# Performance work log

Measured on AMD Instinct MI355X. Metric: run time of the kernel, lower is better.

The kernel has to match this reference:

```python
import jax, jax.numpy as jnp
import numpy as np

D_MODEL = 1024
N_HEADS = 16
D_HEAD = D_MODEL // N_HEADS


def setup_inputs() -> dict:
    key = jax.random.key(0)
    kx, kq, kk, kv = jax.random.split(key, 4)
    B, T = 2, 2048
    X = jax.random.normal(kx, (B, T, D_MODEL), dtype=jnp.float32)
    s = 1.0 / np.sqrt(D_MODEL)
    # torch nn.Linear weight is [out, in]; y = x @ W.T
    Wq = jax.random.uniform(kq, (D_MODEL, D_MODEL), jnp.float32, -s, s)
    Wk = jax.random.uniform(kk, (D_MODEL, D_MODEL), jnp.float32, -s, s)
    Wv = jax.random.uniform(kv, (D_MODEL, D_MODEL), jnp.float32, -s, s)
    return {"X": X, "Wq": Wq, "Wk": Wk, "Wv": Wv}


def reference(X, Wq, Wk, Wv):
    B, T, _ = X.shape
    def heads(W):
        # x @ W.T -> [B,T,D] -> [B,H,T,Dh]
        return (X @ W.T).reshape(B, T, N_HEADS, D_HEAD).transpose(0, 2, 1, 3)
    Q, K, V = heads(Wq), heads(Wk), heads(Wv)
    scores = jnp.einsum('bhqd,bhkd->bhqk', Q, K)
    causal = jnp.tril(jnp.ones((T, T), dtype=bool))
    # original masks with -inf BEFORE scaling; -inf/scale == -inf, so equivalent
    scores = jnp.where(causal, scores, -jnp.inf) / jnp.sqrt(jnp.float32(D_HEAD))
    attn = jax.nn.softmax(scores, axis=-1)
    out = jnp.einsum('bhqk,bhkd->bhqd', attn, V)
    return out.transpose(0, 2, 1, 3).reshape(B, T, N_HEADS * D_HEAD)
```

## Files before the change

kernel.cpp:

```cpp
#include <hip/hip_runtime.h>


using bf16x8   = __attribute__((ext_vector_type(8))) __bf16;
using floatx4  = __attribute__((ext_vector_type(4))) float;
using floatx16 = __attribute__((ext_vector_type(16))) float;
using uintx4   = __attribute__((ext_vector_type(4))) unsigned int;

#define T_SEQ   2048
#define D_MODEL 1024
#define N_HEADS 16
#define D_HEAD  64
#define BATCH   2
#define M_TOT   4096
#define N_TOT   3072
#define PLANE   (T_SEQ * D_HEAD)
#define NX      (M_TOT * D_MODEL)
#define NWSEG   (D_MODEL * D_MODEL)
#define QSCALE  0.18033688f
#define SM_BIAS 24.0f

__device__ __forceinline__ unsigned short f32_to_bf16(float f) {
  unsigned int u = __float_as_uint(f);
  u += 0x7fffu + ((u >> 16) & 1u);
  return (unsigned short)(u >> 16);
}
__device__ __forceinline__ unsigned int pack2_bf16(float a, float b) {
  unsigned int ua = __float_as_uint(a) + 0x8000u;
  unsigned int ub = __float_as_uint(b) + 0x8000u;
  return __builtin_amdgcn_perm(ub, ua, 0x07060302);
}
__device__ __forceinline__ void async_cp16(void* lds, const void* gptr) {
  __builtin_amdgcn_global_load_lds(
      (const __attribute__((address_space(1))) unsigned int*)gptr,
      (__attribute__((address_space(3))) unsigned int*)lds, 16, 0, 0);
}

__global__ __launch_bounds__(256) void cvt_kernel(
    const float* __restrict__ X,  const float* __restrict__ Wq,
    const float* __restrict__ Wk, const float* __restrict__ Wv,
    unsigned short* __restrict__ Xb, unsigned short* __restrict__ Wb)
{
  const size_t i = ((size_t)blockIdx.x * 256 + threadIdx.x) * 8;
  const float* src;
  unsigned short* dst;
  if (i < NX) { src = X + i; dst = Xb + i; }
  else {
    const size_t r = i - NX;
    const int w = (int)(r >> 20);
    const size_t o = r & (NWSEG - 1);
    src = ((w == 0) ? Wq : (w == 1) ? Wk : Wv) + o;
    dst = Wb + r;
  }
  float4 f0 = *(const float4*)src;
  float4 f1 = *(const float4*)(src + 4);
  uint4 out;
  out.x = pack2_bf16(f0.x, f0.y);
  out.y = pack2_bf16(f0.z, f0.w);
  out.z = pack2_bf16(f1.x, f1.y);
  out.w = pack2_bf16(f1.z, f1.w);
  *(uint4*)dst = out;
}

__global__ __launch_bounds__(512, 6) void gemm_qkv(
    const unsigned short* __restrict__ Xb,
    const unsigned short* __restrict__ Wb,
    unsigned short* __restrict__ Qb,
    unsigned short* __restrict__ Kb,
    unsigned short* __restrict__ VTb)
{
  __shared__ unsigned short Als[128 * 64];
  __shared__ unsigned short Bls[128 * 64];

  const int tid  = threadIdx.x;
  const int lane = tid & 63;
  const int wave = tid >> 6;
  const int l15  = lane & 15;
  const int quad = lane >> 4;
  const int wm   = wave & 3;
  const int wn   = wave >> 2;

  const int n_blk = blockIdx.x * 128;
  const int m_blk = blockIdx.y * 128;

  const int swz = (((tid >> 3) ^ tid) & 7) * 8;
  const unsigned short* Ag = Xb + (size_t)(m_blk + (tid >> 3)) * D_MODEL + swz;
  const unsigned short* Bg = Wb + (size_t)(n_blk + (tid >> 3)) * D_MODEL + swz;
  char* Alds = (char*)Als + wave * 1024;
  char* Blds = (char*)Bls + wave * 1024;

  floatx4 acc[2][4] = {};

  for (int k0 = 0; k0 < D_MODEL; k0 += 64) {
    __syncthreads();
#pragma unroll
    for (int p = 0; p < 2; p++) {
      async_cp16(Alds + p * 8192, Ag + (size_t)(p * 64) * D_MODEL + k0);
      async_cp16(Blds + p * 8192, Bg + (size_t)(p * 64) * D_MODEL + k0);
    }
    __syncthreads();

#pragma unroll
    for (int ks = 0; ks < 2; ks++) {
      bf16x8 a[2], b[4];
      const int sa = ((ks * 4 + quad) ^ (l15 & 7)) * 16;
#pragma unroll
      for (int i = 0; i < 2; i++)
        a[i] = *(const bf16x8*)((char*)Als + (wm * 32 + 16 * i + l15) * 128 + sa);
#pragma unroll
      for (int j = 0; j < 4; j++)
        b[j] = *(const bf16x8*)((char*)Bls + (wn * 64 + 16 * j + l15) * 128 + sa);
#pragma unroll
      for (int mi = 0; mi < 2; mi++)
#pragma unroll
        for (int ni = 0; ni < 4; ni++)
          acc[mi][ni] = __builtin_amdgcn_mfma_f32_16x16x32_bf16(a[mi], b[ni], acc[mi][ni], 0, 0, 0);
    }
  }

  __syncthreads();
  char* ep = (char*)Als + wave * 4096;
  const int w_sel  = n_blk >> 10;
  const int m_base = m_blk + wm * 32;
  const int n_base = n_blk + wn * 64;
  const int h      = (n_base & 1023) >> 6;
  const float csc  = (w_sel == 0) ? QSCALE : 1.0f;
  const int bb     = m_base >> 11;

  if (w_sel < 2) {
#pragma unroll
    for (int mi = 0; mi < 2; mi++)
#pragma unroll
      for (int ni = 0; ni < 4; ni++)
#pragma unroll
        for (int r = 0; r < 4; r++) {
          const int row  = 16 * mi + quad * 4 + r;
          const int colb = (16 * ni + l15) * 2;
          const int phys = ((colb >> 4) ^ (row & 7)) * 16;
          *(unsigned short*)(ep + row * 128 + phys + (colb & 15)) =
              f32_to_bf16(acc[mi][ni][r] * csc);
        }
  } else {
#pragma unroll
    for (int mi = 0; mi < 2; mi++)
#pragma unroll
      for (int ni = 0; ni < 4; ni++)
#pragma unroll
        for (int r = 0; r < 4; r++) {
          const int row  = 16 * ni + l15;
          const int colb = (16 * mi + quad * 4 + r) * 2;
          const int phys = ((colb >> 4) ^ (row & 3)) * 16;
          *(unsigned short*)(ep + row * 64 + phys + (colb & 15)) =
              f32_to_bf16(acc[mi][ni][r]);
        }
  }
  asm volatile("s_waitcnt lgkmcnt(0)" ::: "memory");

  if (w_sel < 2) {
#pragma unroll
    for (int pass = 0; pass < 4; pass++) {
      const int row = pass * 8 + (lane >> 3);
      const int cl  = (lane & 7) ^ (row & 7);
      uint4 v = *(const uint4*)(ep + row * 128 + (lane & 7) * 16);
      const int m = m_base + row;
      const int t = m & (T_SEQ - 1);
      unsigned short* dst = ((w_sel == 0) ? Qb : Kb) +
          ((size_t)(bb * N_HEADS + h) * T_SEQ + t) * D_HEAD + cl * 8;
      *(uint4*)dst = v;
    }
  } else {
#pragma unroll
    for (int pass = 0; pass < 4; pass++) {
      const int row = pass * 16 + (lane >> 2);
      const int cl  = (lane & 3) ^ (row & 3);
      uint4 v = *(const uint4*)(ep + row * 64 + (lane & 3) * 16);
      unsigned short* dst = VTb +
          ((size_t)(bb * N_HEADS + h) * D_HEAD + row) * T_SEQ +
          (m_base & (T_SEQ - 1)) + cl * 8;
      *(uint4*)dst = v;
    }
  }
}

__global__ __launch_bounds__(256) void attn_kernel(
    const unsigned short* __restrict__ Qb,
    const unsigned short* __restrict__ Kb,
    const unsigned short* __restrict__ VTb,
    float* __restrict__ Out)
{
  __shared__ __align__(16) char smem[65536];

  const int tid  = threadIdx.x;
  const int lane = tid & 63;
  const int wave = tid >> 6;
  const int l31  = lane & 31;
  const int q1   = lane >> 5;
  const int wq   = wave & 1;
  const int wk   = wave >> 1;

  const int bh   = blockIdx.x & 31;
  const int pair = blockIdx.x >> 5;

  const unsigned short* Qp = Qb  + (size_t)bh * PLANE;
  const unsigned short* Kp = Kb  + (size_t)bh * PLANE;
  const unsigned short* Vp = VTb + (size_t)bh * PLANE;
  const int b = bh >> 4, h = bh & 15;

  const int swz = (((tid >> 3) ^ tid) & 7) * 8;
  const unsigned short* Kg = Kp + (size_t)(tid >> 3) * D_HEAD + swz;
  const unsigned short* Vg = Vp + (size_t)(tid >> 3) * T_SEQ + swz;

  float* const LB = (float*)(smem + 33792);

#define STAGE_CHUNK(c)                                                        \
  do {                                                                        \
    char* kd = smem + (((c) >> 1) & 1) * 16384 + ((c) & 1) * 8192;            \
    char* vd = smem + 32768 + (((c) >> 1) & 1) * 16384 + ((c) & 1) * 8192;    \
    _Pragma("unroll")                                                         \
    for (int p = 0; p < 2; p++) {                                             \
      async_cp16(kd + p * 4096 + wave * 1024,                                 \
                 Kg + (size_t)((c) * 64 + p * 32) * D_HEAD);                  \
      async_cp16(vd + p * 4096 + wave * 1024,                                 \
                 Vg + (size_t)(p * 32) * T_SEQ + (c) * 64);                   \
    }                                                                         \
  } while (0)

#pragma unroll 1
  for (int it = 0; it < 2; it++) {
    const int strip = it ? (31 - pair) : pair;
    const int qbase = strip * 64 + wq * 32;
    const int nch   = strip + 1;

    bf16x8 aq[4];
#pragma unroll
    for (int kp = 0; kp < 4; kp++)
      aq[kp] = *(const bf16x8*)(Qp + (size_t)(qbase + l31) * D_HEAD + kp * 16 + q1 * 8);

    floatx16 o0 = {}, o1 = {};
    float l_acc = 0.0f;

    __syncthreads();

    STAGE_CHUNK(0);
    if (nch > 1) STAGE_CHUNK(1);

#pragma unroll 1
    for (int j2 = 0; j2 < nch; j2 += 2) {
      __syncthreads();
      if (j2 + 2 < nch) STAGE_CHUNK(j2 + 2);

#pragma unroll
      for (int u = 0; u < 2; u++) {
        const int jc = j2 + u;
        if (jc >= nch) break;
        if (u == 1 && j2 + 3 < nch) STAGE_CHUNK(j2 + 3);
        const char* Ksb = smem + ((jc >> 1) & 1) * 16384 + (jc & 1) * 8192;
        const char* Vsb = smem + 32768 + ((jc >> 1) & 1) * 16384 + (jc & 1) * 8192;
        const int kbase = jc * 64 + wk * 32;

        if (kbase <= qbase + 31) {
          floatx16 s = {};
          const int krow = wk * 32 + l31;
          __builtin_amdgcn_s_setprio(1);
#pragma unroll
          for (int kp = 0; kp < 4; kp++) {
            const int c = 2 * kp + q1;
            bf16x8 ak = *(const bf16x8*)(Ksb + krow * 128 + ((c ^ (krow & 7)) * 16));
            s = __builtin_amdgcn_mfma_f32_32x32x16_bf16(ak, aq[kp], s, 0, 0, 0);
          }
          __builtin_amdgcn_s_setprio(0);

          if (kbase >= qbase) {
            const int q = qbase + l31;
#pragma unroll
            for (int r = 0; r < 16; r++) {
              const int kk = kbase + (r & 3) + 8 * (r >> 2) + 4 * q1;
              if (kk > q) s[r] = -INFINITY;
            }
          }

          float pv[16];
#pragma unroll
          for (int r = 0; r < 16; r++)
            pv[r] = __builtin_amdgcn_exp2f(s[r] - SM_BIAS);
#pragma unroll
          for (int r = 0; r < 16; r += 4)
            l_acc += (pv[r] + pv[r + 1]) + (pv[r + 2] + pv[r + 3]);

          unsigned int w[8];
#pragma unroll
          for (int m = 0; m < 8; m++)
            asm("v_cvt_pk_bf16_f32 %0, %1, %2" : "=v"(w[m]) : "v"(pv[2 * m]), "v"(pv[2 * m + 1]));

          __builtin_amdgcn_s_setprio(1);
#pragma unroll
          for (int kp = 0; kp < 2; kp++) {
            unsigned int b0 = w[4 * kp],     b2 = w[4 * kp + 2];
            unsigned int b1 = w[4 * kp + 1], b3 = w[4 * kp + 3];
            asm("v_permlane32_swap_b32 %0, %1" : "+v"(b0), "+v"(b2));
            asm("v_permlane32_swap_b32 %0, %1" : "+v"(b1), "+v"(b3));
            uintx4 uu; uu[0] = b0; uu[1] = b1; uu[2] = b2; uu[3] = b3;
            const bf16x8 pf = __builtin_bit_cast(bf16x8, uu);

            const int cv = 4 * wk + 2 * kp + q1;
            bf16x8 av0 = *(const bf16x8*)(Vsb + l31 * 128 + ((cv ^ (l31 & 7)) * 16));
            o0 = __builtin_amdgcn_mfma_f32_32x32x16_bf16(av0, pf, o0, 0, 0, 0);
            const int row1 = 32 + l31;
            bf16x8 av1 = *(const bf16x8*)(Vsb + row1 * 128 + ((cv ^ (row1 & 7)) * 16));
            o1 = __builtin_amdgcn_mfma_f32_32x32x16_bf16(av1, pf, o1, 0, 0, 0);
          }
          __builtin_amdgcn_s_setprio(0);
        }
      }
    }

    float la = l_acc, lb2 = l_acc;
    asm("v_permlane32_swap_b32 %0, %1" : "+v"(la), "+v"(lb2));
    const float lt = la + lb2;

    __syncthreads();

    float* ob = (float*)smem + (wk * 2 + wq) * (64 * 33);
#pragma unroll
    for (int r = 0; r < 16; r++) {
      const int d0 = (r & 3) + 8 * (r >> 2) + 4 * q1;
      ob[d0 * 33 + l31]        = o0[r];
      ob[(32 + d0) * 33 + l31] = o1[r];
    }
    if (lane < 32) LB[wk * 64 + wq * 32 + l31] = lt;
    __syncthreads();

    const int row = tid >> 2;
    const int dg  = tid & 3;
    const int wqr = row >> 5, ql = row & 31;
    const float inv = 1.0f / (LB[row] + LB[64 + row]);
    const float* obA = (const float*)smem + (0 * 2 + wqr) * (64 * 33);
    const float* obB = (const float*)smem + (1 * 2 + wqr) * (64 * 33);

    float vout[16];
#pragma unroll
    for (int i = 0; i < 16; i++) {
      const int d = dg * 16 + i;
      vout[i] = (obA[d * 33 + ql] + obB[d * 33 + ql]) * inv;
    }
    const int t = strip * 64 + row;
    float* dst = Out + (size_t)(b * T_SEQ + t) * D_MODEL + h * D_HEAD + dg * 16;
#pragma unroll
    for (int m = 0; m < 4; m++)
      *(float4*)(dst + 4 * m) = *(const float4*)(vout + 4 * m);
  }
#undef STAGE_CHUNK
}

extern "C" void kernel_launch(void* const* d_in, const int* in_sizes, int n_in,
                              void* d_out, int out_size, void* d_ws, size_t ws_size,
                              hipStream_t stream) {
  const float* X  = (const float*)d_in[0];
  const float* Wq = (const float*)d_in[1];
  const float* Wk = (const float*)d_in[2];
  const float* Wv = (const float*)d_in[3];

  unsigned short* Qb = (unsigned short*)d_ws;
  unsigned short* Kb = Qb + (size_t)BATCH * N_HEADS * T_SEQ * D_HEAD;
  unsigned short* VT = Kb + (size_t)BATCH * N_HEADS * T_SEQ * D_HEAD;

  unsigned short* Xb = (unsigned short*)d_out;
  unsigned short* Wb = Xb + (size_t)NX;

  cvt_kernel<<<3584, 256, 0, stream>>>(X, Wq, Wk, Wv, Xb, Wb);

  dim3 g1(N_TOT / 128, M_TOT / 128);
  gemm_qkv<<<g1, 512, 0, stream>>>(Xb, Wb, Qb, Kb, VT);

  attn_kernel<<<512, 256, 0, stream>>>(Qb, Kb, VT, (float*)d_out);
}
```

Baseline: 139.8 us.

## Double attention block waves so two KV chunks are processed concurrently

The attention block grows from 256 to 512 threads. The extra four waves handle the second KV chunk of each staged pair in parallel instead of one wave group looping over both chunks serially, and each thread now issues one async copy per chunk instead of two. The partial O accumulators from the two wave groups are summed in shared memory, and the row sums are combined from four partials in the epilogue. This adds latency hiding and parallelism per block, at the cost of more barriers, an extra shared-memory reduction, and possible register pressure under launch_bounds(512,4).

Result: no change. 137.4 us (-1.7%).

```diff
diff --git a/kernel.cpp b/kernel.cpp
--- a/kernel.cpp
+++ b/kernel.cpp
@@ -181,7 +181,7 @@
   }
 }
 
-__global__ __launch_bounds__(256) void attn_kernel(
+__global__ __launch_bounds__(512, 4) void attn_kernel(
     const unsigned short* __restrict__ Qb,
     const unsigned short* __restrict__ Kb,
     const unsigned short* __restrict__ VTb,
@@ -195,7 +195,8 @@
   const int l31  = lane & 31;
   const int q1   = lane >> 5;
   const int wq   = wave & 1;
-  const int wk   = wave >> 1;
+  const int wk   = (wave >> 1) & 1;
+  const int wu   = wave >> 2;
 
   const int bh   = blockIdx.x & 31;
   const int pair = blockIdx.x >> 5;
@@ -205,23 +206,21 @@
   const unsigned short* Vp = VTb + (size_t)bh * PLANE;
   const int b = bh >> 4, h = bh & 15;
 
-  const int swz = (((tid >> 3) ^ tid) & 7) * 8;
-  const unsigned short* Kg = Kp + (size_t)(tid >> 3) * D_HEAD + swz;
-  const unsigned short* Vg = Vp + (size_t)(tid >> 3) * T_SEQ + swz;
+  const int rg = tid >> 3;
+  const int sl = (tid ^ rg) & 7;
+  const unsigned short* Kg = Kp + (size_t)rg * D_HEAD + sl * 8;
+  const unsigned short* Vg = Vp + (size_t)rg * T_SEQ + sl * 8;
 
   float* const LB = (float*)(smem + 33792);
 
 #define STAGE_CHUNK(c)                                                        \
   do {                                                                        \
-    char* kd = smem + (((c) >> 1) & 1) * 16384 + ((c) & 1) * 8192;            \
-    char* vd = smem + 32768 + (((c) >> 1) & 1) * 16384 + ((c) & 1) * 8192;    \
-    _Pragma("unroll")                                                         \
-    for (int p = 0; p < 2; p++) {                                             \
-      async_cp16(kd + p * 4096 + wave * 1024,                                 \
-                 Kg + (size_t)((c) * 64 + p * 32) * D_HEAD);                  \
-      async_cp16(vd + p * 4096 + wave * 1024,                                 \
-                 Vg + (size_t)(p * 32) * T_SEQ + (c) * 64);                   \
-    }                                                                         \
+    char* kd = smem + (((c) >> 1) & 1) * 16384 + ((c) & 1) * 8192             \
+               + wave * 1024;                                                 \
+    char* vd = smem + 32768 + (((c) >> 1) & 1) * 16384 + ((c) & 1) * 8192     \
+               + wave * 1024;                                                 \
+    async_cp16(kd, Kg + (size_t)(c) * (64 * D_HEAD));                         \
+    async_cp16(vd, Vg + (size_t)(c) * 64);                                    \
   } while (0)
 
 #pragma unroll 1
@@ -247,69 +246,66 @@
     for (int j2 = 0; j2 < nch; j2 += 2) {
       __syncthreads();
       if (j2 + 2 < nch) STAGE_CHUNK(j2 + 2);
-
-#pragma unroll
-      for (int u = 0; u < 2; u++) {
-        const int jc = j2 + u;
-        if (jc >= nch) break;
-        if (u == 1 && j2 + 3 < nch) STAGE_CHUNK(j2 + 3);
+      if (j2 + 3 < nch) STAGE_CHUNK(j2 + 3);
+
+      const int jc = j2 + wu;
+      const int kbase = jc * 64 + wk * 32;
+
+      if (jc < nch && kbase <= qbase + 31) {
         const char* Ksb = smem + ((jc >> 1) & 1) * 16384 + (jc & 1) * 8192;
         const char* Vsb = smem + 32768 + ((jc >> 1) & 1) * 16384 + (jc & 1) * 8192;
-        const int kbase = jc * 64 + wk * 32;
-
-        if (kbase <= qbase + 31) {
-          floatx16 s = {};
-          const int krow = wk * 32 + l31;
-          __builtin_amdgcn_s_setprio(1);
-#pragma unroll
-          for (int kp = 0; kp < 4; kp++) {
-            const int c = 2 * kp + q1;
-            bf16x8 ak = *(const bf16x8*)(Ksb + krow * 128 + ((c ^ (krow & 7)) * 16));
-            s = __builtin_amdgcn_mfma_f32_32x32x16_bf16(ak, aq[kp], s, 0, 0, 0);
+
+        floatx16 s = {};
+        const int krow = wk * 32 + l31;
+        __builtin_amdgcn_s_setprio(1);
+#pragma unroll
+        for (int kp = 0; kp < 4; kp++) {
+          const int c = 2 * kp + q1;
+          bf16x8 ak = *(const bf16x8*)(Ksb + krow * 128 + ((c ^ (krow & 7)) * 16));
+          s = __builtin_amdgcn_mfma_f32_32x32x16_bf16(ak, aq[kp], s, 0, 0, 0);
+        }
+        __builtin_amdgcn_s_setprio(0);
+
+        if (kbase >= qbase) {
+          const int q = qbase + l31;
+#pragma unroll
+          for (int r = 0; r < 16; r++) {
+            const int kk = kbase + (r & 3) + 8 * (r >> 2) + 4 * q1;
+            if (kk > q) s[r] = -INFINITY;
           }
-          __builtin_amdgcn_s_setprio(0);
-
-          if (kbase >= qbase) {
-            const int q = qbase + l31;
-#pragma unroll
-            for (int r = 0; r < 16; r++) {
-              const int kk = kbase + (r & 3) + 8 * (r >> 2) + 4 * q1;
-              if (kk > q) s[r] = -INFINITY;
-            }
-          }
-
-          float pv[16];
-#pragma unroll
-          for (int r = 0; r < 16; r++)
-            pv[r] = __builtin_amdgcn_exp2f(s[r] - SM_BIAS);
-#pragma unroll
-          for (int r = 0; r < 16; r += 4)
-            l_acc += (pv[r] + pv[r + 1]) + (pv[r + 2] + pv[r + 3]);
-
-          unsigned int w[8];
-#pragma unroll
-          for (int m = 0; m < 8; m++)
-            asm("v_cvt_pk_bf16_f32 %0, %1, %2" : "=v"(w[m]) : "v"(pv[2 * m]), "v"(pv[2 * m + 1]));
-
-          __builtin_amdgcn_s_setprio(1);
-#pragma unroll
-          for (int kp = 0; kp < 2; kp++) {
-            unsigned int b0 = w[4 * kp],     b2 = w[4 * kp + 2];
-            unsigned int b1 = w[4 * kp + 1], b3 = w[4 * kp + 3];
-            asm("v_permlane32_swap_b32 %0, %1" : "+v"(b0), "+v"(b2));
-            asm("v_permlane32_swap_b32 %0, %1" : "+v"(b1), "+v"(b3));
-            uintx4 uu; uu[0] = b0; uu[1] = b1; uu[2] = b2; uu[3] = b3;
-            const bf16x8 pf = __builtin_bit_cast(bf16x8, uu);
-
-            const int cv = 4 * wk + 2 * kp + q1;
-            bf16x8 av0 = *(const bf16x8*)(Vsb + l31 * 128 + ((cv ^ (l31 & 7)) * 16));
-            o0 = __builtin_amdgcn_mfma_f32_32x32x16_bf16(av0, pf, o0, 0, 0, 0);
-            const int row1 = 32 + l31;
-            bf16x8 av1 = *(const bf16x8*)(Vsb + row1 * 128 + ((cv ^ (row1 & 7)) * 16));
-            o1 = __builtin_amdgcn_mfma_f32_32x32x16_bf16(av1, pf, o1, 0, 0, 0);
-          }
-          __builtin_amdgcn_s_setprio(0);
-        }
+        }
+
+        float pv[16];
+#pragma unroll
+        for (int r = 0; r < 16; r++)
+          pv[r] = __builtin_amdgcn_exp2f(s[r] - SM_BIAS);
+#pragma unroll
+        for (int r = 0; r < 16; r += 4)
+          l_acc += (pv[r] + pv[r + 1]) + (pv[r + 2] + pv[r + 3]);
+
+        unsigned int w[8];
+#pragma unroll
+        for (int m = 0; m < 8; m++)
+          asm("v_cvt_pk_bf16_f32 %0, %1, %2" : "=v"(w[m]) : "v"(pv[2 * m]), "v"(pv[2 * m + 1]));
+
+        __builtin_amdgcn_s_setprio(1);
+#pragma unroll
+        for (int kp = 0; kp < 2; kp++) {
+          unsigned int b0 = w[4 * kp],     b2 = w[4 * kp + 2];
+          unsigned int b1 = w[4 * kp + 1], b3 = w[4 * kp + 3];
+          asm("v_permlane32_swap_b32 %0, %1" : "+v"(b0), "+v"(b2));
+          asm("v_permlane32_swap_b32 %0, %1" : "+v"(b1), "+v"(b3));
+          uintx4 uu; uu[0] = b0; uu[1] = b1; uu[2] = b2; uu[3] = b3;
+          const bf16x8 pf = __builtin_bit_cast(bf16x8, uu);
+
+          const int cv = 4 * wk + 2 * kp + q1;
+          bf16x8 av0 = *(const bf16x8*)(Vsb + l31 * 128 + ((cv ^ (l31 & 7)) * 16));
+          o0 = __builtin_amdgcn_mfma_f32_32x32x16_bf16(av0, pf, o0, 0, 0, 0);
+          const int row1 = 32 + l31;
+          bf16x8 av1 = *(const bf16x8*)(Vsb + row1 * 128 + ((cv ^ (row1 & 7)) * 16));
+          o1 = __builtin_amdgcn_mfma_f32_32x32x16_bf16(av1, pf, o1, 0, 0, 0);
+        }
+        __builtin_amdgcn_s_setprio(0);
       }
     }
 
@@ -320,33 +316,45 @@
     __syncthreads();
 
     float* ob = (float*)smem + (wk * 2 + wq) * (64 * 33);
-#pragma unroll
-    for (int r = 0; r < 16; r++) {
-      const int d0 = (r & 3) + 8 * (r >> 2) + 4 * q1;
-      ob[d0 * 33 + l31]        = o0[r];
-      ob[(32 + d0) * 33 + l31] = o1[r];
-    }
-    if (lane < 32) LB[wk * 64 + wq * 32 + l31] = lt;
-    __syncthreads();
-
-    const int row = tid >> 2;
-    const int dg  = tid & 3;
+    if (wu == 0) {
+#pragma unroll
+      for (int r = 0; r < 16; r++) {
+        const int d0 = (r & 3) + 8 * (r >> 2) + 4 * q1;
+        ob[d0 * 33 + l31]        = o0[r];
+        ob[(32 + d0) * 33 + l31] = o1[r];
+      }
+    }
+    if (lane < 32) LB[wave * 32 + l31] = lt;
+    __syncthreads();
+    if (wu == 1) {
+#pragma unroll
+      for (int r = 0; r < 16; r++) {
+        const int d0 = (r & 3) + 8 * (r >> 2) + 4 * q1;
+        ob[d0 * 33 + l31]        += o0[r];
+        ob[(32 + d0) * 33 + l31] += o1[r];
+      }
+    }
+    __syncthreads();
+
+    const int row = tid >> 3;
+    const int dg  = tid & 7;
     const int wqr = row >> 5, ql = row & 31;
-    const float inv = 1.0f / (LB[row] + LB[64 + row]);
-    const float* obA = (const float*)smem + (0 * 2 + wqr) * (64 * 33);
-    const float* obB = (const float*)smem + (1 * 2 + wqr) * (64 * 33);
-
-    float vout[16];
-#pragma unroll
-    for (int i = 0; i < 16; i++) {
-      const int d = dg * 16 + i;
-      vout[i] = (obA[d * 33 + ql] + obB[d * 33 + ql]) * inv;
+    const float lsum = (LB[wqr * 32 + ql]       + LB[(wqr + 2) * 32 + ql]) +
+                       (LB[(wqr + 4) * 32 + ql] + LB[(wqr + 6) * 32 + ql]);
+    const float inv = 1.0f / lsum;
+    const float* p0 = (const float*)smem + (0 * 2 + wqr) * (64 * 33);
+    const float* p1 = (const float*)smem + (1 * 2 + wqr) * (64 * 33);
+
+    float vout[8];
+#pragma unroll
+    for (int i = 0; i < 8; i++) {
+      const int d = dg * 8 + i;
+      vout[i] = (p0[d * 33 + ql] + p1[d * 33 + ql]) * inv;
     }
     const int t = strip * 64 + row;
-    float* dst = Out + (size_t)(b * T_SEQ + t) * D_MODEL + h * D_HEAD + dg * 16;
-#pragma unroll
-    for (int m = 0; m < 4; m++)
-      *(float4*)(dst + 4 * m) = *(const float4*)(vout + 4 * m);
+    float* dst = Out + (size_t)(b * T_SEQ + t) * D_MODEL + h * D_HEAD + dg * 8;
+    *(float4*)(dst)     = *(const float4*)(vout);
+    *(float4*)(dst + 4) = *(const float4*)(vout + 4);
   }
 #undef STAGE_CHUNK
 }
@@ -371,5 +379,5 @@
   dim3 g1(N_TOT / 128, M_TOT / 128);
   gemm_qkv<<<g1, 512, 0, stream>>>(Xb, Wb, Qb, Kb, VT);
 
-  attn_kernel<<<512, 256, 0, stream>>>(Qb, Kb, VT, (float*)d_out);
-}
+  attn_kernel<<<512, 512, 0, stream>>>(Qb, Kb, VT, (float*)d_out);
+}
```
